# Kernel optimization log

Measured on AMD Instinct MI355X. Metric: run time of the kernel, lower is better.

## Reference

```python
import jax, jax.numpy as jnp
import numpy as np
from jax import lax

CHUNK = 32

def _l2norm(x, eps=1e-6):
    # matches fla l2norm: x / ||x||_2 along last dim
    return x * lax.rsqrt(jnp.sum(x * x, axis=-1, keepdims=True) + eps)

def _delta_rule_chunkwise(q, k, v, beta, chunk=CHUNK):
    b, h, L, dk = q.shape
    dv = v.shape[-1]
    pad = (-L) % chunk
    if pad:
        pw = ((0, 0), (0, 0), (0, pad), (0, 0))
        q = jnp.pad(q, pw); k = jnp.pad(k, pw); v = jnp.pad(v, pw)
        beta = jnp.pad(beta, ((0, 0), (0, 0), (0, pad)))
    Lp = L + pad
    n = Lp // chunk

    q = _l2norm(q)
    k = _l2norm(k)
    v = v * beta[..., None]
    k_beta = k * beta[..., None]

    # [b,h,n,c,d]
    rs = lambda t: t.reshape(b, h, n, chunk, t.shape[-1])
    qc, kc, vc, kbc = rs(q), rs(k), rs(v), rs(k_beta)

    idx = jnp.arange(chunk)
    strict_lower = (idx[:, None] > idx[None, :])           # used for inv
    lower_incl = (idx[:, None] >= idx[None, :])            # used for attn_local

    # inv = -(k_beta k^T), keep strictly-lower part only
    inv = jnp.where(strict_lower, -jnp.einsum('bhnid,bhnjd->bhnij', kbc, kc), 0.0)
    # sequential forward substitution: inv[i,:i] += inv[i,:] @ inv[:,:i]
    for i in range(1, chunk):
        row = inv[..., i, :]                                # [b,h,n,c]
        upd = jnp.einsum('bhnk,bhnkc->bhnc', row, inv)      # contributions from rows < i
        inv = inv.at[..., i, :].add(jnp.where(idx < i, upd, 0.0))
    inv = inv + jnp.eye(chunk, dtype=inv.dtype)

    u = jnp.einsum('bhnij,bhnjd->bhnid', inv, vc)           # [b,h,n,c,dv]
    w = jnp.einsum('bhnij,bhnjd->bhnid', inv, kbc)          # [b,h,n,c,dk]

    S0 = jnp.zeros((b, h, dk, dv), dtype=q.dtype)

    def step(S, blk):
        q_i, k_i, u_i0, w_i = blk
        attn = jnp.where(lower_incl, jnp.einsum('bhid,bhjd->bhij', q_i, k_i), 0.0)
        u_i = u_i0 - jnp.einsum('bhik,bhkd->bhid', w_i, S)
        o = jnp.einsum('bhik,bhkd->bhid', q_i, S) + jnp.einsum('bhij,bhjd->bhid', attn, u_i)
        S = S + jnp.einsum('bhci,bhcd->bhid', k_i, u_i)
        return S, o

    mv = lambda t: jnp.moveaxis(t, 2, 0)                    # [n,b,h,c,d]
    S, outs = lax.scan(step, S0, (mv(qc), mv(kc), mv(u), mv(w)))
    out = jnp.moveaxis(outs, 0, 2).reshape(b, h, Lp, dv)
    if pad:
        out = out[:, :, :L]
    return out, S

def setup_inputs() -> dict:
    key = jax.random.key(0)
    kq, kk, kv, kb = jax.random.split(key, 4)
    b, h, L, d = 2, 16, 4096, 128
    q = jax.random.normal(kq, (b, h, L, d), dtype=jnp.float32)
    k = jax.random.normal(kk, (b, h, L, d), dtype=jnp.float32)
    v = jax.random.normal(kv, (b, h, L, d), dtype=jnp.float32)
    beta = jax.random.uniform(kb, (b, h, L), dtype=jnp.float32)
    return {"q": q, "k": k, "v": v, "beta": beta}

def reference(q, k, v, beta):
    return _delta_rule_chunkwise(q, k, v, beta)
```

## Files before the change

### kernel.cpp

```cpp
#include <hip/hip_runtime.h>
#include <math.h>

#define BH   32
#define LSEQ 4096
#define DK   128
#define DV   128
#define CH   32
#define NC   (LSEQ/CH)

typedef float4 f4;
typedef unsigned short u16;
typedef __attribute__((ext_vector_type(8))) short  bf16x8;
typedef __attribute__((ext_vector_type(4))) float  f32x4;

#define MFMA16(a,b,c) __builtin_amdgcn_mfma_f32_16x16x32_bf16((a),(b),(c),0,0,0)

__device__ __forceinline__ float dot4(const f4 a, const f4 b) {
    return a.x*b.x + a.y*b.y + a.z*b.z + a.w*b.w;
}
__device__ __forceinline__ unsigned pk2(float a, float b) {
    unsigned ua = __builtin_bit_cast(unsigned, a);
    unsigned ub = __builtin_bit_cast(unsigned, b);
    ua = (ua + 0x7FFFu + ((ua >> 16) & 1u)) >> 16;
    ub = (ub + 0x7FFFu + ((ub >> 16) & 1u)) >> 16;
    return (ua & 0xFFFFu) | (ub << 16);
}
__device__ __forceinline__ u16 bf1(float a) {
    unsigned ua = __builtin_bit_cast(unsigned, a);
    ua = (ua + 0x7FFFu + ((ua >> 16) & 1u)) >> 16;
    return (u16)ua;
}

__global__ __launch_bounds__(256) void prep_kernel(
    const float* __restrict__ q, const float* __restrict__ k, float* __restrict__ v,
    const float* __restrict__ beta,
    u16* __restrict__ qb16, u16* __restrict__ wb16,
    u16* __restrict__ kT16, u16* __restrict__ A16)
{
    __shared__ u16 qn[CH][136];
    __shared__ u16 kn[CH][136];
    __shared__ u16 vT[DK][40];
    __shared__ u16 knT[DK][40];
    __shared__ float Ts[CH][33];
    __shared__ float Af[CH][33];
    __shared__ u16 Tb[CH][40];
    __shared__ float redq[CH][8], redk[CH][8];
    __shared__ float bet[CH], scq[CH], sck[CH];

    const int tid = threadIdx.x;
    const int hh  = blockIdx.x >> 7;
    const int c   = blockIdx.x & (NC-1);
    const size_t rowbase = (size_t)hh * LSEQ + (size_t)c * CH;
    const size_t base    = rowbase * DK;
    const size_t tb      = (size_t)(hh * NC + c);

    const int r = tid >> 3, sub = tid & 7, d0 = sub * 16;
    const int wid = tid >> 6, lane = tid & 63, quad = lane >> 4, m16 = lane & 15;

    f4 tq[4], tk[4], tv[4];
    float sq = 0.f, sk = 0.f;
#pragma unroll
    for (int m = 0; m < 4; ++m) {
        tq[m] = *(const f4*)(q + base + (size_t)r*DK + d0 + m*4);
        tk[m] = *(const f4*)(k + base + (size_t)r*DK + d0 + m*4);
        tv[m] = *(const f4*)(v + base + (size_t)r*DK + d0 + m*4);
        sq += dot4(tq[m], tq[m]);
        sk += dot4(tk[m], tk[m]);
    }
    redq[r][sub] = sq;
    redk[r][sub] = sk;
    if (tid < CH) bet[tid] = beta[rowbase + tid];
    __syncthreads();
    if (tid < CH) {
        float a = 0.f, b = 0.f;
#pragma unroll
        for (int j = 0; j < 8; ++j) { a += redq[tid][j]; b += redk[tid][j]; }
        scq[tid] = 1.0f / sqrtf(a + 1e-6f);
        sck[tid] = 1.0f / sqrtf(b + 1e-6f);
    }
    __syncthreads();
    const float aq = scq[r], ak = sck[r];
#pragma unroll
    for (int m = 0; m < 4; ++m) {
        tq[m].x *= aq; tq[m].y *= aq; tq[m].z *= aq; tq[m].w *= aq;
        tk[m].x *= ak; tk[m].y *= ak; tk[m].z *= ak; tk[m].w *= ak;
    }
    {
        uint4 p0, p1;
        p0.x = pk2(tq[0].x,tq[0].y); p0.y = pk2(tq[0].z,tq[0].w);
        p0.z = pk2(tq[1].x,tq[1].y); p0.w = pk2(tq[1].z,tq[1].w);
        p1.x = pk2(tq[2].x,tq[2].y); p1.y = pk2(tq[2].z,tq[2].w);
        p1.z = pk2(tq[3].x,tq[3].y); p1.w = pk2(tq[3].z,tq[3].w);
        *(uint4*)&qn[r][d0]     = p0;  *(uint4*)&qn[r][d0+8] = p1;
        *(uint4*)(qb16 + tb*4096 + (size_t)r*DK + d0)     = p0;
        *(uint4*)(qb16 + tb*4096 + (size_t)r*DK + d0 + 8) = p1;
        uint4 k0, k1;
        k0.x = pk2(tk[0].x,tk[0].y); k0.y = pk2(tk[0].z,tk[0].w);
        k0.z = pk2(tk[1].x,tk[1].y); k0.w = pk2(tk[1].z,tk[1].w);
        k1.x = pk2(tk[2].x,tk[2].y); k1.y = pk2(tk[2].z,tk[2].w);
        k1.z = pk2(tk[3].x,tk[3].y); k1.w = pk2(tk[3].z,tk[3].w);
        *(uint4*)&kn[r][d0]     = k0;  *(uint4*)&kn[r][d0+8] = k1;
    }
#pragma unroll
    for (int m = 0; m < 4; ++m) {
        knT[d0+m*4+0][r] = bf1(tk[m].x); knT[d0+m*4+1][r] = bf1(tk[m].y);
        knT[d0+m*4+2][r] = bf1(tk[m].z); knT[d0+m*4+3][r] = bf1(tk[m].w);
        vT [d0+m*4+0][r] = bf1(tv[m].x); vT [d0+m*4+1][r] = bf1(tv[m].y);
        vT [d0+m*4+2][r] = bf1(tv[m].z); vT [d0+m*4+3][r] = bf1(tv[m].w);
    }
    __syncthreads();

    {
        const int d = tid >> 1, jh = (tid & 1) * 16;
        uint4 z0 = *(const uint4*)&knT[d][jh];
        uint4 z1 = *(const uint4*)&knT[d][jh+8];
        *(uint4*)(kT16 + tb*4096 + (size_t)d*32 + jh)     = z0;
        *(uint4*)(kT16 + tb*4096 + (size_t)d*32 + jh + 8) = z1;
    }
    {
        const int ti = wid >> 1, tj = wid & 1;
        f32x4 aA = {0.f,0.f,0.f,0.f}, aG = {0.f,0.f,0.f,0.f};
#pragma unroll
        for (int ks = 0; ks < 4; ++ks) {
            bf16x8 xq = *(const bf16x8*)&qn[ti*16+m16][ks*32 + quad*8];
            bf16x8 xk = *(const bf16x8*)&kn[ti*16+m16][ks*32 + quad*8];
            bf16x8 yk = *(const bf16x8*)&kn[tj*16+m16][ks*32 + quad*8];
            aA = MFMA16(xq, yk, aA);
            aG = MFMA16(xk, yk, aG);
        }
#pragma unroll
        for (int reg = 0; reg < 4; ++reg) {
            Af[ti*16 + quad*4 + reg][tj*16 + m16] = aA[reg];
            Ts[ti*16 + quad*4 + reg][tj*16 + m16] = aG[reg];
        }
    }
    __syncthreads();

    {
        const int i = r, j0 = sub * 4;
        float a[4];
#pragma unroll
        for (int jj = 0; jj < 4; ++jj)
            a[jj] = (j0+jj <= i) ? Af[i][j0+jj] : 0.f;
        uint2 pa; pa.x = pk2(a[0], a[1]); pa.y = pk2(a[2], a[3]);
        *(uint2*)(A16 + tb*1024 + (size_t)i*32 + j0) = pa;
        const float bi = bet[i];
#pragma unroll
        for (int jj = 0; jj < 4; ++jj) {
            const int j = j0 + jj;
            const float gv = Ts[i][j];
            Ts[i][j] = (j < i) ? -bi * gv : 0.f;
        }
    }
    __syncthreads();

    if (tid < 32) {
        float rr[32];
#pragma unroll
        for (int i = 0; i < 32; ++i) rr[i] = Ts[i][tid];
#pragma unroll
        for (int i = 1; i < 32; ++i) {
            float t = 0.f;
#pragma unroll
            for (int kk = 0; kk < i; ++kk)
                t += __shfl(rr[i], kk) * rr[kk];
            rr[i] += t;
        }
        const float bj = bet[tid];
#pragma unroll
        for (int i = 0; i < 32; ++i)
            Ts[i][tid] = ((i == tid) ? 1.0f : rr[i]) * bj;
    }
    __syncthreads();
    {
        const int i = r, j0 = sub * 4;
        uint2 p; p.x = pk2(Ts[i][j0], Ts[i][j0+1]); p.y = pk2(Ts[i][j0+2], Ts[i][j0+3]);
        *(uint2*)&Tb[i][j0] = p;
    }
    __syncthreads();

#pragma unroll
    for (int dt = 0; dt < 2; ++dt)
#pragma unroll
    for (int it = 0; it < 2; ++it) {
        const int drow = wid*32 + dt*16 + m16;
        bf16x8 av  = *(const bf16x8*)&vT[drow][quad*8];
        bf16x8 ak2 = *(const bf16x8*)&knT[drow][quad*8];
        bf16x8 bT  = *(const bf16x8*)&Tb[it*16 + m16][quad*8];
        f32x4 aU = {0.f,0.f,0.f,0.f}, aW = {0.f,0.f,0.f,0.f};
        aU = MFMA16(av,  bT, aU);
        aW = MFMA16(ak2, bT, aW);
        const int ii = it*16 + m16;
        const int dd = wid*32 + dt*16 + quad*4;
        f4 us; us.x = aU[0]; us.y = aU[1]; us.z = aU[2]; us.w = aU[3];
        *(f4*)(v + base + (size_t)ii*DK + dd) = us;
        uint2 pw; pw.x = pk2(-aW[0], -aW[1]); pw.y = pk2(-aW[2], -aW[3]);
        *(uint2*)(wb16 + tb*4096 + (size_t)ii*DK + dd) = pw;
    }
}

__global__ __launch_bounds__(256) void scan_kernel(
    const u16* __restrict__ qb16, const u16* __restrict__ wb16,
    const u16* __restrict__ kT16, const u16* __restrict__ A16,
    const float* __restrict__ u0, float* __restrict__ out)
{
    __shared__ u16 qb[2][CH][136];
    __shared__ u16 wb[2][CH][136];
    __shared__ u16 kT[DK][40];
    __shared__ u16 Ab[CH][40];
    __shared__ u16 ST[16][136];
    __shared__ u16 uT[16][40];

    const int tid  = threadIdx.x;
    const int hh   = blockIdx.x & (BH-1);
    const int g    = blockIdx.x >> 5;
    const int wid  = tid >> 6;
    const int lane = tid & 63;
    const int quad = lane >> 4;
    const int m16  = lane & 15;

    const int srow = tid >> 3, sd0 = (tid & 7) * 16;
    const int kd = tid >> 1, kjh = (tid & 1) * 16;
    const int aj = (tid & 7) * 4;

    for (int i = tid; i < 16*136; i += 256) ((u16*)ST)[i] = 0;

    f32x4 S0 = {0.f,0.f,0.f,0.f}, S1 = {0.f,0.f,0.f,0.f};

    uint4 pq0, pq1, pw0, pw1, pk0, pk1; uint2 pa;
    float pu0 = 0.f, pu1 = 0.f, pu2 = 0.f, pu3 = 0.f;
    {
        const size_t tb = (size_t)(hh * NC);
        const u16* qg = qb16 + tb*4096;
        const u16* wg = wb16 + tb*4096;
        const u16* kg = kT16 + tb*4096;
        const u16* Ag = A16  + tb*1024;
        pq0 = *(const uint4*)(qg + (size_t)srow*DK + sd0);
        pq1 = *(const uint4*)(qg + (size_t)srow*DK + sd0 + 8);
        pw0 = *(const uint4*)(wg + (size_t)srow*DK + sd0);
        pw1 = *(const uint4*)(wg + (size_t)srow*DK + sd0 + 8);
        pk0 = *(const uint4*)(kg + (size_t)kd*32 + kjh);
        pk1 = *(const uint4*)(kg + (size_t)kd*32 + kjh + 8);
        pa  = *(const uint2*)(Ag + (size_t)srow*32 + aj);
        if (wid < 2) {
            const float* up = u0 + ((size_t)hh*LSEQ + wid*16 + quad*4)*DK + g*16 + m16;
            pu0 = up[0]; pu1 = up[DK]; pu2 = up[2*DK]; pu3 = up[3*DK];
        }
    }
    __syncthreads();

    for (int c = 0; c < NC; ++c) {
        const int buf = c & 1;
        *(uint4*)&qb[buf][srow][sd0]   = pq0;  *(uint4*)&qb[buf][srow][sd0+8] = pq1;
        *(uint4*)&wb[buf][srow][sd0]   = pw0;  *(uint4*)&wb[buf][srow][sd0+8] = pw1;
        __syncthreads();
        *(uint4*)&kT[kd][kjh]  = pk0;  *(uint4*)&kT[kd][kjh+8] = pk1;
        *(uint2*)&Ab[srow][aj] = pa;

        f32x4 acc;
        if (wid < 2) { acc.x = pu0; acc.y = pu1; acc.z = pu2; acc.w = pu3; }
        else         { acc.x = 0.f; acc.y = 0.f; acc.z = 0.f; acc.w = 0.f; }

        if (c + 1 < NC) {
            const size_t tb = (size_t)(hh*NC + c + 1);
            const u16* qg = qb16 + tb*4096;
            const u16* wg = wb16 + tb*4096;
            const u16* kg = kT16 + tb*4096;
            const u16* Ag = A16  + tb*1024;
            pq0 = *(const uint4*)(qg + (size_t)srow*DK + sd0);
            pq1 = *(const uint4*)(qg + (size_t)srow*DK + sd0 + 8);
            pw0 = *(const uint4*)(wg + (size_t)srow*DK + sd0);
            pw1 = *(const uint4*)(wg + (size_t)srow*DK + sd0 + 8);
            pk0 = *(const uint4*)(kg + (size_t)kd*32 + kjh);
            pk1 = *(const uint4*)(kg + (size_t)kd*32 + kjh + 8);
            pa  = *(const uint2*)(Ag + (size_t)srow*32 + aj);
            if (wid < 2) {
                const float* up = u0 + ((size_t)hh*LSEQ + (size_t)(c+1)*CH + wid*16 + quad*4)*DK
                                     + g*16 + m16;
                pu0 = up[0]; pu1 = up[DK]; pu2 = up[2*DK]; pu3 = up[3*DK];
            }
        }

        if (wid < 2) {
#pragma unroll
            for (int ks = 0; ks < 4; ++ks) {
                bf16x8 af = *(const bf16x8*)&wb[buf][wid*16 + m16][ks*32 + quad*8];
                bf16x8 bf = *(const bf16x8*)&ST[m16][ks*32 + quad*8];
                acc = MFMA16(af, bf, acc);
            }
            uint2 p; p.x = pk2(acc.x, acc.y); p.y = pk2(acc.z, acc.w);
            *(uint2*)&uT[m16][wid*16 + quad*4] = p;
        } else {
            const int tile = wid - 2;
#pragma unroll
            for (int ks = 0; ks < 4; ++ks) {
                bf16x8 af = *(const bf16x8*)&qb[buf][tile*16 + m16][ks*32 + quad*8];
                bf16x8 bf = *(const bf16x8*)&ST[m16][ks*32 + quad*8];
                acc = MFMA16(af, bf, acc);
            }
        }
        __syncthreads();

        bf16x8 ub = *(const bf16x8*)&uT[m16][quad*8];
        if (wid >= 2) {
            const int tile = wid - 2;
            bf16x8 af = *(const bf16x8*)&Ab[tile*16 + m16][quad*8];
            acc = MFMA16(af, ub, acc);
            float* op = out + ((size_t)hh*LSEQ + (size_t)c*CH + tile*16 + quad*4)*DV
                            + g*16 + m16;
            op[0] = acc.x; op[DV] = acc.y; op[2*DV] = acc.z; op[3*DV] = acc.w;
        }
        {
            bf16x8 a0 = *(const bf16x8*)&kT[wid*32 + m16][quad*8];
            bf16x8 a1 = *(const bf16x8*)&kT[wid*32 + 16 + m16][quad*8];
            S0 = MFMA16(a0, ub, S0);
            S1 = MFMA16(a1, ub, S1);
            uint2 p0; p0.x = pk2(S0.x, S0.y); p0.y = pk2(S0.z, S0.w);
            uint2 p1; p1.x = pk2(S1.x, S1.y); p1.y = pk2(S1.z, S1.w);
            *(uint2*)&ST[m16][wid*32 + quad*4]      = p0;
            *(uint2*)&ST[m16][wid*32 + 16 + quad*4] = p1;
        }
        __syncthreads();
    }

    {
        float* sp = out + (size_t)BH*LSEQ*DV
                        + ((size_t)hh*DK + wid*32 + quad*4)*DV + g*16 + m16;
        sp[0] = S0.x; sp[DV] = S0.y; sp[2*DV] = S0.z; sp[3*DV] = S0.w;
        float* sq = sp + (size_t)16*DV;
        sq[0] = S1.x; sq[DV] = S1.y; sq[2*DV] = S1.z; sq[3*DV] = S1.w;
    }
}

extern "C" void kernel_launch(void* const* d_in, const int* in_sizes, int n_in,
                              void* d_out, int out_size, void* d_ws, size_t ws_size,
                              hipStream_t stream) {
    (void)in_sizes; (void)n_in; (void)out_size; (void)ws_size;
    const float* q = (const float*)d_in[0];
    const float* k = (const float*)d_in[1];
    float* v = (float*)d_in[2];
    const float* beta = (const float*)d_in[3];
    float* out = (float*)d_out;

    const size_t NE = (size_t)BH * LSEQ * DK;
    u16* qb16 = (u16*)d_ws;
    u16* wb16 = qb16 + NE;
    u16* kT16 = wb16 + NE;
    u16* A16  = kT16 + NE;

    prep_kernel<<<dim3(BH*NC), dim3(256), 0, stream>>>(q, k, v, beta, qb16, wb16, kT16, A16);
    scan_kernel<<<dim3(8*BH), dim3(256), 0, stream>>>(qb16, wb16, kT16, A16, v, out);
}
```

Baseline: 395.2 us.

## Restructure scan kernel to one barrier per chunk with register-resident fragments

The sequential chunk scan is rewritten so every wave recomputes the u correction redundantly and passes it between lanes with shuffles rather than through LDS. This cuts the per-chunk barriers from three to one. The k and q/A fragments are loaded straight from global memory into registers one chunk ahead, and the w and u tiles are prefetched three chunks ahead into double-buffered, swizzled LDS. Only two waves now hold the state S, four tiles each. In exchange the u MFMAs are duplicated across all four waves, register pressure rises, and launch_bounds caps occupancy at one block.

```diff
diff --git a/kernel.cpp b/kernel.cpp
--- a/kernel.cpp
+++ b/kernel.cpp
@@ -199,17 +199,14 @@
     }
 }
 
-__global__ __launch_bounds__(256) void scan_kernel(
+__global__ __launch_bounds__(256, 1) void scan_kernel(
     const u16* __restrict__ qb16, const u16* __restrict__ wb16,
     const u16* __restrict__ kT16, const u16* __restrict__ A16,
     const float* __restrict__ u0, float* __restrict__ out)
 {
-    __shared__ u16 qb[2][CH][136];
-    __shared__ u16 wb[2][CH][136];
-    __shared__ u16 kT[DK][40];
-    __shared__ u16 Ab[CH][40];
-    __shared__ u16 ST[16][136];
-    __shared__ u16 uT[16][40];
+    __shared__ u16   wbc[2][16][CH][8];
+    __shared__ u16   STc[2][16][16][8];
+    __shared__ float uIT[2][16][36];
 
     const int tid  = threadIdx.x;
     const int hh   = blockIdx.x & (BH-1);
@@ -219,117 +216,148 @@
     const int quad = lane >> 4;
     const int m16  = lane & 15;
 
-    const int srow = tid >> 3, sd0 = (tid & 7) * 16;
-    const int kd = tid >> 1, kjh = (tid & 1) * 16;
-    const int aj = (tid & 7) * 4;
-
-    for (int i = tid; i < 16*136; i += 256) ((u16*)ST)[i] = 0;
-
+    const int srow = tid >> 3;
+    const int spl  = (tid & 7) * 2;
+    const int um   = (tid & 7) * 2;
+
+    const u16* qg = qb16 + (size_t)hh * NC * 4096;
+    const u16* wg = wb16 + (size_t)hh * NC * 4096;
+    const u16* kg = kT16 + (size_t)hh * NC * 4096;
+    const u16* Ag = A16  + (size_t)hh * NC * 1024;
+    const float* ug = u0 + (size_t)hh * LSEQ * DK + g * 16;
+
+    uint4 Ow0, Ow1, Ew0, Ew1; float2 Ou, Eu;
+    bf16x8 F0 = {}, F1 = {}, F2 = {}, F3 = {}, AF = {};
     f32x4 S0 = {0.f,0.f,0.f,0.f}, S1 = {0.f,0.f,0.f,0.f};
-
-    uint4 pq0, pq1, pw0, pw1, pk0, pk1; uint2 pa;
-    float pu0 = 0.f, pu1 = 0.f, pu2 = 0.f, pu3 = 0.f;
-    {
-        const size_t tb = (size_t)(hh * NC);
-        const u16* qg = qb16 + tb*4096;
-        const u16* wg = wb16 + tb*4096;
-        const u16* kg = kT16 + tb*4096;
-        const u16* Ag = A16  + tb*1024;
-        pq0 = *(const uint4*)(qg + (size_t)srow*DK + sd0);
-        pq1 = *(const uint4*)(qg + (size_t)srow*DK + sd0 + 8);
-        pw0 = *(const uint4*)(wg + (size_t)srow*DK + sd0);
-        pw1 = *(const uint4*)(wg + (size_t)srow*DK + sd0 + 8);
-        pk0 = *(const uint4*)(kg + (size_t)kd*32 + kjh);
-        pk1 = *(const uint4*)(kg + (size_t)kd*32 + kjh + 8);
-        pa  = *(const uint2*)(Ag + (size_t)srow*32 + aj);
-        if (wid < 2) {
-            const float* up = u0 + ((size_t)hh*LSEQ + wid*16 + quad*4)*DK + g*16 + m16;
-            pu0 = up[0]; pu1 = up[DK]; pu2 = up[2*DK]; pu3 = up[3*DK];
-        }
-    }
-    __syncthreads();
-
-    for (int c = 0; c < NC; ++c) {
-        const int buf = c & 1;
-        *(uint4*)&qb[buf][srow][sd0]   = pq0;  *(uint4*)&qb[buf][srow][sd0+8] = pq1;
-        *(uint4*)&wb[buf][srow][sd0]   = pw0;  *(uint4*)&wb[buf][srow][sd0+8] = pw1;
-        __syncthreads();
-        *(uint4*)&kT[kd][kjh]  = pk0;  *(uint4*)&kT[kd][kjh+8] = pk1;
-        *(uint2*)&Ab[srow][aj] = pa;
-
-        f32x4 acc;
-        if (wid < 2) { acc.x = pu0; acc.y = pu1; acc.z = pu2; acc.w = pu3; }
-        else         { acc.x = 0.f; acc.y = 0.f; acc.z = 0.f; acc.w = 0.f; }
-
-        if (c + 1 < NC) {
-            const size_t tb = (size_t)(hh*NC + c + 1);
-            const u16* qg = qb16 + tb*4096;
-            const u16* wg = wb16 + tb*4096;
-            const u16* kg = kT16 + tb*4096;
-            const u16* Ag = A16  + tb*1024;
-            pq0 = *(const uint4*)(qg + (size_t)srow*DK + sd0);
-            pq1 = *(const uint4*)(qg + (size_t)srow*DK + sd0 + 8);
-            pw0 = *(const uint4*)(wg + (size_t)srow*DK + sd0);
-            pw1 = *(const uint4*)(wg + (size_t)srow*DK + sd0 + 8);
-            pk0 = *(const uint4*)(kg + (size_t)kd*32 + kjh);
-            pk1 = *(const uint4*)(kg + (size_t)kd*32 + kjh + 8);
-            pa  = *(const uint2*)(Ag + (size_t)srow*32 + aj);
-            if (wid < 2) {
-                const float* up = u0 + ((size_t)hh*LSEQ + (size_t)(c+1)*CH + wid*16 + quad*4)*DK
-                                     + g*16 + m16;
-                pu0 = up[0]; pu1 = up[DK]; pu2 = up[2*DK]; pu3 = up[3*DK];
-            }
-        }
-
-        if (wid < 2) {
-#pragma unroll
-            for (int ks = 0; ks < 4; ++ks) {
-                bf16x8 af = *(const bf16x8*)&wb[buf][wid*16 + m16][ks*32 + quad*8];
-                bf16x8 bf = *(const bf16x8*)&ST[m16][ks*32 + quad*8];
-                acc = MFMA16(af, bf, acc);
-            }
-            uint2 p; p.x = pk2(acc.x, acc.y); p.y = pk2(acc.z, acc.w);
-            *(uint2*)&uT[m16][wid*16 + quad*4] = p;
-        } else {
-            const int tile = wid - 2;
-#pragma unroll
-            for (int ks = 0; ks < 4; ++ks) {
-                bf16x8 af = *(const bf16x8*)&qb[buf][tile*16 + m16][ks*32 + quad*8];
-                bf16x8 bf = *(const bf16x8*)&ST[m16][ks*32 + quad*8];
-                acc = MFMA16(af, bf, acc);
-            }
-        }
-        __syncthreads();
-
-        bf16x8 ub = *(const bf16x8*)&uT[m16][quad*8];
-        if (wid >= 2) {
-            const int tile = wid - 2;
-            bf16x8 af = *(const bf16x8*)&Ab[tile*16 + m16][quad*8];
-            acc = MFMA16(af, ub, acc);
-            float* op = out + ((size_t)hh*LSEQ + (size_t)c*CH + tile*16 + quad*4)*DV
-                            + g*16 + m16;
-            op[0] = acc.x; op[DV] = acc.y; op[2*DV] = acc.z; op[3*DV] = acc.w;
-        }
-        {
-            bf16x8 a0 = *(const bf16x8*)&kT[wid*32 + m16][quad*8];
-            bf16x8 a1 = *(const bf16x8*)&kT[wid*32 + 16 + m16][quad*8];
-            S0 = MFMA16(a0, ub, S0);
-            S1 = MFMA16(a1, ub, S1);
-            uint2 p0; p0.x = pk2(S0.x, S0.y); p0.y = pk2(S0.z, S0.w);
-            uint2 p1; p1.x = pk2(S1.x, S1.y); p1.y = pk2(S1.z, S1.w);
-            *(uint2*)&ST[m16][wid*32 + quad*4]      = p0;
-            *(uint2*)&ST[m16][wid*32 + 16 + quad*4] = p1;
-        }
-        __syncthreads();
-    }
-
-    {
+    f32x4 S2 = {0.f,0.f,0.f,0.f}, S3 = {0.f,0.f,0.f,0.f};
+
+#define PREF(P, cc) do { \
+    const u16* wp_ = wg + (size_t)(cc)*4096 + (size_t)srow*DK + (tid&7)*16; \
+    P##w0 = *(const uint4*)(wp_); \
+    P##w1 = *(const uint4*)(wp_ + 8); \
+    P##u  = *(const float2*)(ug + ((size_t)(cc)*CH + srow)*DK + um); \
+} while (0)
+
+#define STAGE(P, nb_) do { \
+    *(uint4*)&wbc[nb_][spl  ][srow][0] = P##w0; \
+    *(uint4*)&wbc[nb_][spl+1][srow][0] = P##w1; \
+    uIT[nb_][um  ][srow] = P##u.x; \
+    uIT[nb_][um+1][srow] = P##u.y; \
+} while (0)
+
+#define LOADFRAGS(cc) do { \
+    if (wid < 2) { \
+        const u16* kp_ = kg + (size_t)(cc)*4096 + (size_t)(wid*64 + m16)*32 + quad*8; \
+        F0 = *(const bf16x8*)(kp_); \
+        F1 = *(const bf16x8*)(kp_ + 16*32); \
+        F2 = *(const bf16x8*)(kp_ + 32*32); \
+        F3 = *(const bf16x8*)(kp_ + 48*32); \
+    } else { \
+        const u16* qp_ = qg + (size_t)(cc)*4096 + (size_t)((wid-2)*16 + m16)*DK + quad*8; \
+        F0 = *(const bf16x8*)(qp_); \
+        F1 = *(const bf16x8*)(qp_ + 32); \
+        F2 = *(const bf16x8*)(qp_ + 64); \
+        F3 = *(const bf16x8*)(qp_ + 96); \
+        AF = *(const bf16x8*)(Ag + (size_t)(cc)*1024 + (size_t)((wid-2)*16 + m16)*32 + quad*8); \
+    } \
+} while (0)
+
+    for (int i = tid; i < 16*16*8; i += 256) (&STc[0][0][0][0])[i] = 0;
+    PREF(O, 0);
+    STAGE(O, 0);
+    PREF(O, 1);
+    PREF(E, 2);
+    LOADFRAGS(0);
+    __syncthreads();
+
+#define BODY(c, b, P) do { \
+    const int nb = (b) ^ 1; \
+    STAGE(P, nb); \
+    { const int c3_ = ((c)+3 < NC) ? (c)+3 : NC-1; PREF(P, c3_); } \
+     \
+    f32x4 u0a = *(const f32x4*)&uIT[b][m16][quad*4]; \
+    f32x4 u1a = *(const f32x4*)&uIT[b][m16][16 + quad*4]; \
+    f32x4 u0b = {0.f,0.f,0.f,0.f}, u1b = {0.f,0.f,0.f,0.f}; \
+    bf16x8 sf0 = *(const bf16x8*)&STc[b][quad    ][m16][0]; \
+    bf16x8 sf1 = *(const bf16x8*)&STc[b][ 4+quad ][m16][0]; \
+    bf16x8 sf2 = *(const bf16x8*)&STc[b][ 8+quad ][m16][0]; \
+    bf16x8 sf3 = *(const bf16x8*)&STc[b][12+quad ][m16][0]; \
+    u0a = MFMA16(*(const bf16x8*)&wbc[b][quad    ][   m16][0], sf0, u0a); \
+    u1a = MFMA16(*(const bf16x8*)&wbc[b][quad    ][16+m16][0], sf0, u1a); \
+    u0b = MFMA16(*(const bf16x8*)&wbc[b][ 4+quad ][   m16][0], sf1, u0b); \
+    u1b = MFMA16(*(const bf16x8*)&wbc[b][ 4+quad ][16+m16][0], sf1, u1b); \
+    u0a = MFMA16(*(const bf16x8*)&wbc[b][ 8+quad ][   m16][0], sf2, u0a); \
+    u1a = MFMA16(*(const bf16x8*)&wbc[b][ 8+quad ][16+m16][0], sf2, u1a); \
+    u0b = MFMA16(*(const bf16x8*)&wbc[b][12+quad ][   m16][0], sf3, u0b); \
+    u1b = MFMA16(*(const bf16x8*)&wbc[b][12+quad ][16+m16][0], sf3, u1b); \
+    u0a[0]+=u0b[0]; u0a[1]+=u0b[1]; u0a[2]+=u0b[2]; u0a[3]+=u0b[3]; \
+    u1a[0]+=u1b[0]; u1a[1]+=u1b[1]; u1a[2]+=u1b[2]; u1a[3]+=u1b[3]; \
+     \
+    const unsigned W00 = pk2(u0a[0], u0a[1]), W01 = pk2(u0a[2], u0a[3]); \
+    const unsigned W10 = pk2(u1a[0], u1a[1]), W11 = pk2(u1a[2], u1a[3]); \
+    const int s0l_ = (2*(quad&1))*16 + m16, s1l_ = s0l_ + 16; \
+    union { unsigned w[4]; bf16x8 v; } uc_; \
+    { const unsigned a0_ = __shfl((int)W00, s0l_), b0_ = __shfl((int)W10, s0l_); \
+      const unsigned a1_ = __shfl((int)W01, s0l_), b1_ = __shfl((int)W11, s0l_); \
+      const unsigned a2_ = __shfl((int)W00, s1l_), b2_ = __shfl((int)W10, s1l_); \
+      const unsigned a3_ = __shfl((int)W01, s1l_), b3_ = __shfl((int)W11, s1l_); \
+      const bool hi_ = (quad >= 2); \
+      uc_.w[0] = hi_ ? b0_ : a0_; uc_.w[1] = hi_ ? b1_ : a1_; \
+      uc_.w[2] = hi_ ? b2_ : a2_; uc_.w[3] = hi_ ? b3_ : a3_; } \
+    const bf16x8 ub_ = uc_.v; \
+    if (wid < 2) { \
+         \
+        const int db_ = wid * 64; \
+        S0 = MFMA16(F0, ub_, S0); \
+        S1 = MFMA16(F1, ub_, S1); \
+        S2 = MFMA16(F2, ub_, S2); \
+        S3 = MFMA16(F3, ub_, S3); \
+        uint2 p_; \
+        p_.x = pk2(S0[0],S0[1]); p_.y = pk2(S0[2],S0[3]); \
+        *(uint2*)&STc[nb][(db_>>3)   + (quad>>1)][m16][4*(quad&1)] = p_; \
+        p_.x = pk2(S1[0],S1[1]); p_.y = pk2(S1[2],S1[3]); \
+        *(uint2*)&STc[nb][(db_>>3)+2 + (quad>>1)][m16][4*(quad&1)] = p_; \
+        p_.x = pk2(S2[0],S2[1]); p_.y = pk2(S2[2],S2[3]); \
+        *(uint2*)&STc[nb][(db_>>3)+4 + (quad>>1)][m16][4*(quad&1)] = p_; \
+        p_.x = pk2(S3[0],S3[1]); p_.y = pk2(S3[2],S3[3]); \
+        *(uint2*)&STc[nb][(db_>>3)+6 + (quad>>1)][m16][4*(quad&1)] = p_; \
+    } else { \
+         \
+        f32x4 Za = {0.f,0.f,0.f,0.f}, Zb = {0.f,0.f,0.f,0.f}; \
+        Za = MFMA16(F0, sf0, Za); \
+        Zb = MFMA16(F1, sf1, Zb); \
+        Za = MFMA16(F2, sf2, Za); \
+        Zb = MFMA16(F3, sf3, Zb); \
+        Za[0]+=Zb[0]; Za[1]+=Zb[1]; Za[2]+=Zb[2]; Za[3]+=Zb[3]; \
+        Za = MFMA16(AF, ub_, Za); \
+        float* op_ = out + ((size_t)hh*LSEQ + (size_t)(c)*CH + (wid-2)*16 + quad*4)*DV \
+                         + g*16 + m16; \
+        op_[0] = Za[0]; op_[DV] = Za[1]; op_[2*DV] = Za[2]; op_[3*DV] = Za[3]; \
+    } \
+    { const int c1_ = ((c)+1 < NC) ? (c)+1 : NC-1; LOADFRAGS(c1_); } \
+    __syncthreads(); \
+} while (0)
+
+    for (int c = 0; c < NC; c += 2) {
+        BODY(c,     0, O);
+        BODY(c + 1, 1, E);
+    }
+
+    if (wid < 2) {
         float* sp = out + (size_t)BH*LSEQ*DV
-                        + ((size_t)hh*DK + wid*32 + quad*4)*DV + g*16 + m16;
-        sp[0] = S0.x; sp[DV] = S0.y; sp[2*DV] = S0.z; sp[3*DV] = S0.w;
-        float* sq = sp + (size_t)16*DV;
-        sq[0] = S1.x; sq[DV] = S1.y; sq[2*DV] = S1.z; sq[3*DV] = S1.w;
-    }
+                        + ((size_t)hh*DK + wid*64 + quad*4)*DV + g*16 + m16;
+        sp[0] = S0[0]; sp[DV] = S0[1]; sp[2*DV] = S0[2]; sp[3*DV] = S0[3];
+        sp += (size_t)16*DV;
+        sp[0] = S1[0]; sp[DV] = S1[1]; sp[2*DV] = S1[2]; sp[3*DV] = S1[3];
+        sp += (size_t)16*DV;
+        sp[0] = S2[0]; sp[DV] = S2[1]; sp[2*DV] = S2[2]; sp[3*DV] = S2[3];
+        sp += (size_t)16*DV;
+        sp[0] = S3[0]; sp[DV] = S3[1]; sp[2*DV] = S3[2]; sp[3*DV] = S3[3];
+    }
+#undef BODY
+#undef LOADFRAGS
+#undef STAGE
+#undef PREF
 }
 
 extern "C" void kernel_launch(void* const* d_in, const int* in_sizes, int n_in,
```

New measurement: 378.3 us. -4.3%, faster.

## Rewrite scan as single-wave blocks using register fragments and MFMA-ready layouts

Applied to the files above, without the earlier changes.

The prep kernel now writes q, w, kT and A in a pre-swizzled MFMA fragment order, so the scan kernel can load operands straight into registers with contiguous per-lane loads. The scan kernel drops to one 64-thread wave per block. It keeps the state S in accumulator registers, shares u across lanes with shuffles, and round-trips only S through a small swizzled LDS buffer, which removes all block-wide barriers from the sequential chunk loop. It also prefetches the next chunk's fragments between MFMA groups and uses the hardware bf16 pack instruction. The trade-off is higher register pressure and only 4x fewer threads per block to cover memory latency.

```diff
diff --git a/kernel.cpp b/kernel.cpp
--- a/kernel.cpp
+++ b/kernel.cpp
@@ -29,6 +29,11 @@
     unsigned ua = __builtin_bit_cast(unsigned, a);
     ua = (ua + 0x7FFFu + ((ua >> 16) & 1u)) >> 16;
     return (u16)ua;
+}
+__device__ __forceinline__ unsigned cvtpk(float a, float b) {
+    unsigned r;
+    asm("v_cvt_pk_bf16_f32 %0, %1, %2" : "=v"(r) : "v"(a), "v"(b));
+    return r;
 }
 
 __global__ __launch_bounds__(256) void prep_kernel(
@@ -92,8 +97,9 @@
         p1.x = pk2(tq[2].x,tq[2].y); p1.y = pk2(tq[2].z,tq[2].w);
         p1.z = pk2(tq[3].x,tq[3].y); p1.w = pk2(tq[3].z,tq[3].w);
         *(uint4*)&qn[r][d0]     = p0;  *(uint4*)&qn[r][d0+8] = p1;
-        *(uint4*)(qb16 + tb*4096 + (size_t)r*DK + d0)     = p0;
-        *(uint4*)(qb16 + tb*4096 + (size_t)r*DK + d0 + 8) = p1;
+        const int qf = ((r>>4)*4 + (sub>>1))*512 + ((r&15) + (sub&1)*32)*8;
+        *(uint4*)(qb16 + tb*4096 + qf)       = p0;
+        *(uint4*)(qb16 + tb*4096 + qf + 128) = p1;
         uint4 k0, k1;
         k0.x = pk2(tk[0].x,tk[0].y); k0.y = pk2(tk[0].z,tk[0].w);
         k0.z = pk2(tk[1].x,tk[1].y); k0.w = pk2(tk[1].z,tk[1].w);
@@ -114,8 +120,9 @@
         const int d = tid >> 1, jh = (tid & 1) * 16;
         uint4 z0 = *(const uint4*)&knT[d][jh];
         uint4 z1 = *(const uint4*)&knT[d][jh+8];
-        *(uint4*)(kT16 + tb*4096 + (size_t)d*32 + jh)     = z0;
-        *(uint4*)(kT16 + tb*4096 + (size_t)d*32 + jh + 8) = z1;
+        const int kf = (d>>4)*512 + ((d&15) + (tid&1)*32)*8;
+        *(uint4*)(kT16 + tb*4096 + kf)       = z0;
+        *(uint4*)(kT16 + tb*4096 + kf + 128) = z1;
     }
     {
         const int ti = wid >> 1, tj = wid & 1;
@@ -143,7 +150,8 @@
         for (int jj = 0; jj < 4; ++jj)
             a[jj] = (j0+jj <= i) ? Af[i][j0+jj] : 0.f;
         uint2 pa; pa.x = pk2(a[0], a[1]); pa.y = pk2(a[2], a[3]);
-        *(uint2*)(A16 + tb*1024 + (size_t)i*32 + j0) = pa;
+        const int af = (i>>4)*512 + ((i&15) + (sub>>1)*16)*8 + (sub&1)*4;
+        *(uint2*)(A16 + tb*1024 + af) = pa;
         const float bi = bet[i];
 #pragma unroll
         for (int jj = 0; jj < 4; ++jj) {
@@ -195,141 +203,142 @@
         f4 us; us.x = aU[0]; us.y = aU[1]; us.z = aU[2]; us.w = aU[3];
         *(f4*)(v + base + (size_t)ii*DK + dd) = us;
         uint2 pw; pw.x = pk2(-aW[0], -aW[1]); pw.y = pk2(-aW[2], -aW[3]);
-        *(uint2*)(wb16 + tb*4096 + (size_t)ii*DK + dd) = pw;
-    }
-}
-
-__global__ __launch_bounds__(256) void scan_kernel(
+        const int wf = (it*4 + wid)*512 + (m16 + (dt*2 + (quad>>1))*16)*8 + (quad&1)*4;
+        *(uint2*)(wb16 + tb*4096 + wf) = pw;
+    }
+}
+
+__global__ __launch_bounds__(64) void scan_kernel(
     const u16* __restrict__ qb16, const u16* __restrict__ wb16,
     const u16* __restrict__ kT16, const u16* __restrict__ A16,
     const float* __restrict__ u0, float* __restrict__ out)
 {
-    __shared__ u16 qb[2][CH][136];
-    __shared__ u16 wb[2][CH][136];
-    __shared__ u16 kT[DK][40];
-    __shared__ u16 Ab[CH][40];
-    __shared__ u16 ST[16][136];
-    __shared__ u16 uT[16][40];
-
-    const int tid  = threadIdx.x;
-    const int hh   = blockIdx.x & (BH-1);
-    const int g    = blockIdx.x >> 5;
-    const int wid  = tid >> 6;
-    const int lane = tid & 63;
-    const int quad = lane >> 4;
-    const int m16  = lane & 15;
-
-    const int srow = tid >> 3, sd0 = (tid & 7) * 16;
-    const int kd = tid >> 1, kjh = (tid & 1) * 16;
-    const int aj = (tid & 7) * 4;
-
-    for (int i = tid; i < 16*136; i += 256) ((u16*)ST)[i] = 0;
-
-    f32x4 S0 = {0.f,0.f,0.f,0.f}, S1 = {0.f,0.f,0.f,0.f};
-
-    uint4 pq0, pq1, pw0, pw1, pk0, pk1; uint2 pa;
-    float pu0 = 0.f, pu1 = 0.f, pu2 = 0.f, pu3 = 0.f;
-    {
-        const size_t tb = (size_t)(hh * NC);
-        const u16* qg = qb16 + tb*4096;
-        const u16* wg = wb16 + tb*4096;
-        const u16* kg = kT16 + tb*4096;
-        const u16* Ag = A16  + tb*1024;
-        pq0 = *(const uint4*)(qg + (size_t)srow*DK + sd0);
-        pq1 = *(const uint4*)(qg + (size_t)srow*DK + sd0 + 8);
-        pw0 = *(const uint4*)(wg + (size_t)srow*DK + sd0);
-        pw1 = *(const uint4*)(wg + (size_t)srow*DK + sd0 + 8);
-        pk0 = *(const uint4*)(kg + (size_t)kd*32 + kjh);
-        pk1 = *(const uint4*)(kg + (size_t)kd*32 + kjh + 8);
-        pa  = *(const uint2*)(Ag + (size_t)srow*32 + aj);
-        if (wid < 2) {
-            const float* up = u0 + ((size_t)hh*LSEQ + wid*16 + quad*4)*DK + g*16 + m16;
-            pu0 = up[0]; pu1 = up[DK]; pu2 = up[2*DK]; pu3 = up[3*DK];
-        }
-    }
-    __syncthreads();
+    __shared__ u16 STl[16*128];
+
+    const int lane = threadIdx.x;
+    const int quad = lane >> 4, m16 = lane & 15;
+    const int hh = blockIdx.x & 31, g = blockIdx.x >> 5;
+
+    const u16* wg = wb16 + (size_t)hh * NC * 4096 + lane*8;
+    const u16* qg = qb16 + (size_t)hh * NC * 4096 + lane*8;
+    const u16* kg = kT16 + (size_t)hh * NC * 4096 + lane*8;
+    const u16* Ag = A16  + (size_t)hh * NC * 1024 + lane*8;
+    const float* ug = u0 + (size_t)hh * LSEQ * DK + (size_t)(quad*4)*DK + g*16 + m16;
+    float* og = out + (size_t)hh * LSEQ * DV + (size_t)(quad*4)*DV + g*16 + m16;
+
+    const int swz = (m16 & 7) << 3;
+
+    bf16x8 WA[8], KA[8], QA[8], AA[2];
+    f32x4 U0r[2];
+    f32x4 SA[8];
+    bf16x8 SB[4];
+#pragma unroll
+    for (int t = 0; t < 8; ++t) SA[t] = (f32x4){0.f,0.f,0.f,0.f};
+#pragma unroll
+    for (int ks = 0; ks < 4; ++ks) SB[ks] = (bf16x8){};
+
+#define LOADWU(cc) do { \
+    const u16* wp_ = wg + (size_t)(cc)*4096; \
+    _Pragma("unroll") \
+    for (int f = 0; f < 8; ++f) WA[f] = *(const bf16x8*)(wp_ + f*512); \
+    const float* up_ = ug + (size_t)(cc)*CH*DK; \
+    _Pragma("unroll") \
+    for (int r2 = 0; r2 < 4; ++r2) { \
+        U0r[0][r2] = up_[(size_t)r2*DK]; \
+        U0r[1][r2] = up_[(size_t)(16+r2)*DK]; } \
+} while (0)
+#define LOADK(cc) do { \
+    const u16* kp_ = kg + (size_t)(cc)*4096; \
+    _Pragma("unroll") \
+    for (int f = 0; f < 8; ++f) KA[f] = *(const bf16x8*)(kp_ + f*512); \
+} while (0)
+#define LOADQ(cc) do { \
+    const u16* qp_ = qg + (size_t)(cc)*4096; \
+    _Pragma("unroll") \
+    for (int f = 0; f < 8; ++f) QA[f] = *(const bf16x8*)(qp_ + f*512); \
+    const u16* ap_ = Ag + (size_t)(cc)*1024; \
+    AA[0] = *(const bf16x8*)(ap_); \
+    AA[1] = *(const bf16x8*)(ap_ + 512); \
+} while (0)
+
+    LOADWU(0); LOADK(0); LOADQ(0);
 
     for (int c = 0; c < NC; ++c) {
-        const int buf = c & 1;
-        *(uint4*)&qb[buf][srow][sd0]   = pq0;  *(uint4*)&qb[buf][srow][sd0+8] = pq1;
-        *(uint4*)&wb[buf][srow][sd0]   = pw0;  *(uint4*)&wb[buf][srow][sd0+8] = pw1;
-        __syncthreads();
-        *(uint4*)&kT[kd][kjh]  = pk0;  *(uint4*)&kT[kd][kjh+8] = pk1;
-        *(uint2*)&Ab[srow][aj] = pa;
-
-        f32x4 acc;
-        if (wid < 2) { acc.x = pu0; acc.y = pu1; acc.z = pu2; acc.w = pu3; }
-        else         { acc.x = 0.f; acc.y = 0.f; acc.z = 0.f; acc.w = 0.f; }
-
-        if (c + 1 < NC) {
-            const size_t tb = (size_t)(hh*NC + c + 1);
-            const u16* qg = qb16 + tb*4096;
-            const u16* wg = wb16 + tb*4096;
-            const u16* kg = kT16 + tb*4096;
-            const u16* Ag = A16  + tb*1024;
-            pq0 = *(const uint4*)(qg + (size_t)srow*DK + sd0);
-            pq1 = *(const uint4*)(qg + (size_t)srow*DK + sd0 + 8);
-            pw0 = *(const uint4*)(wg + (size_t)srow*DK + sd0);
-            pw1 = *(const uint4*)(wg + (size_t)srow*DK + sd0 + 8);
-            pk0 = *(const uint4*)(kg + (size_t)kd*32 + kjh);
-            pk1 = *(const uint4*)(kg + (size_t)kd*32 + kjh + 8);
-            pa  = *(const uint2*)(Ag + (size_t)srow*32 + aj);
-            if (wid < 2) {
-                const float* up = u0 + ((size_t)hh*LSEQ + (size_t)(c+1)*CH + wid*16 + quad*4)*DK
-                                     + g*16 + m16;
-                pu0 = up[0]; pu1 = up[DK]; pu2 = up[2*DK]; pu3 = up[3*DK];
-            }
-        }
-
-        if (wid < 2) {
-#pragma unroll
-            for (int ks = 0; ks < 4; ++ks) {
-                bf16x8 af = *(const bf16x8*)&wb[buf][wid*16 + m16][ks*32 + quad*8];
-                bf16x8 bf = *(const bf16x8*)&ST[m16][ks*32 + quad*8];
-                acc = MFMA16(af, bf, acc);
-            }
-            uint2 p; p.x = pk2(acc.x, acc.y); p.y = pk2(acc.z, acc.w);
-            *(uint2*)&uT[m16][wid*16 + quad*4] = p;
-        } else {
-            const int tile = wid - 2;
-#pragma unroll
-            for (int ks = 0; ks < 4; ++ks) {
-                bf16x8 af = *(const bf16x8*)&qb[buf][tile*16 + m16][ks*32 + quad*8];
-                bf16x8 bf = *(const bf16x8*)&ST[m16][ks*32 + quad*8];
-                acc = MFMA16(af, bf, acc);
-            }
-        }
-        __syncthreads();
-
-        bf16x8 ub = *(const bf16x8*)&uT[m16][quad*8];
-        if (wid >= 2) {
-            const int tile = wid - 2;
-            bf16x8 af = *(const bf16x8*)&Ab[tile*16 + m16][quad*8];
-            acc = MFMA16(af, ub, acc);
-            float* op = out + ((size_t)hh*LSEQ + (size_t)c*CH + tile*16 + quad*4)*DV
-                            + g*16 + m16;
-            op[0] = acc.x; op[DV] = acc.y; op[2*DV] = acc.z; op[3*DV] = acc.w;
-        }
+        const int cn = (c + 1 < NC) ? c + 1 : c;
+
+        f32x4 ua0 = U0r[0], ua1 = U0r[1];
+        f32x4 ub0 = {0.f,0.f,0.f,0.f}, ub1 = {0.f,0.f,0.f,0.f};
+        ua0 = MFMA16(WA[0], SB[0], ua0);  ub0 = MFMA16(WA[1], SB[1], ub0);
+        ua0 = MFMA16(WA[2], SB[2], ua0);  ub0 = MFMA16(WA[3], SB[3], ub0);
+        ua1 = MFMA16(WA[4], SB[0], ua1);  ub1 = MFMA16(WA[5], SB[1], ub1);
+        ua1 = MFMA16(WA[6], SB[2], ua1);  ub1 = MFMA16(WA[7], SB[3], ub1);
+        ua0 += ub0;  ua1 += ub1;
+
+        LOADWU(cn);
+
+        const unsigned Wa0 = cvtpk(ua0[0], ua0[1]), Wa1 = cvtpk(ua0[2], ua0[3]);
+        const unsigned Wb0 = cvtpk(ua1[0], ua1[1]), Wb1 = cvtpk(ua1[2], ua1[3]);
+        const int s0l = ((quad & 1) << 5) + m16, s1l = s0l + 16;
+        union { unsigned w[4]; bf16x8 v; } uc;
         {
-            bf16x8 a0 = *(const bf16x8*)&kT[wid*32 + m16][quad*8];
-            bf16x8 a1 = *(const bf16x8*)&kT[wid*32 + 16 + m16][quad*8];
-            S0 = MFMA16(a0, ub, S0);
-            S1 = MFMA16(a1, ub, S1);
-            uint2 p0; p0.x = pk2(S0.x, S0.y); p0.y = pk2(S0.z, S0.w);
-            uint2 p1; p1.x = pk2(S1.x, S1.y); p1.y = pk2(S1.z, S1.w);
-            *(uint2*)&ST[m16][wid*32 + quad*4]      = p0;
-            *(uint2*)&ST[m16][wid*32 + 16 + quad*4] = p1;
-        }
-        __syncthreads();
-    }
-
-    {
-        float* sp = out + (size_t)BH*LSEQ*DV
-                        + ((size_t)hh*DK + wid*32 + quad*4)*DV + g*16 + m16;
-        sp[0] = S0.x; sp[DV] = S0.y; sp[2*DV] = S0.z; sp[3*DV] = S0.w;
-        float* sq = sp + (size_t)16*DV;
-        sq[0] = S1.x; sq[DV] = S1.y; sq[2*DV] = S1.z; sq[3*DV] = S1.w;
-    }
+            const unsigned a0 = __shfl((int)Wa0, s0l), b0 = __shfl((int)Wb0, s0l);
+            const unsigned a1 = __shfl((int)Wa1, s0l), b1 = __shfl((int)Wb1, s0l);
+            const unsigned a2 = __shfl((int)Wa0, s1l), b2 = __shfl((int)Wb0, s1l);
+            const unsigned a3 = __shfl((int)Wa1, s1l), b3 = __shfl((int)Wb1, s1l);
+            const bool hi = (quad >= 2);
+            uc.w[0] = hi ? b0 : a0; uc.w[1] = hi ? b1 : a1;
+            uc.w[2] = hi ? b2 : a2; uc.w[3] = hi ? b3 : a3;
+        }
+        const bf16x8 UB = uc.v;
+
+#pragma unroll
+        for (int t = 0; t < 8; ++t)
+            SA[t] = MFMA16(KA[t], UB, SA[t]);
+
+        LOADK(cn);
+
+        f32x4 za0 = {0.f,0.f,0.f,0.f}, zb0 = {0.f,0.f,0.f,0.f};
+        f32x4 za1 = {0.f,0.f,0.f,0.f}, zb1 = {0.f,0.f,0.f,0.f};
+        za0 = MFMA16(QA[0], SB[0], za0);  zb0 = MFMA16(QA[1], SB[1], zb0);
+        za0 = MFMA16(QA[2], SB[2], za0);  zb0 = MFMA16(QA[3], SB[3], zb0);
+        za1 = MFMA16(QA[4], SB[0], za1);  zb1 = MFMA16(QA[5], SB[1], zb1);
+        za1 = MFMA16(QA[6], SB[2], za1);  zb1 = MFMA16(QA[7], SB[3], zb1);
+        za0 += zb0;  za1 += zb1;
+        za0 = MFMA16(AA[0], UB, za0);
+        za1 = MFMA16(AA[1], UB, za1);
+        {
+            float* o0 = og + (size_t)c * CH * DV;
+            o0[0] = za0[0]; o0[DV] = za0[1]; o0[2*DV] = za0[2]; o0[3*DV] = za0[3];
+            float* o1 = o0 + (size_t)16 * DV;
+            o1[0] = za1[0]; o1[DV] = za1[1]; o1[2*DV] = za1[2]; o1[3*DV] = za1[3];
+        }
+
+        LOADQ(cn);
+
+#pragma unroll
+        for (int t = 0; t < 8; ++t) {
+            uint2 p;
+            p.x = cvtpk(SA[t][0], SA[t][1]);
+            p.y = cvtpk(SA[t][2], SA[t][3]);
+            *(uint2*)&STl[(m16*128 + t*16 + quad*4) ^ swz] = p;
+        }
+#pragma unroll
+        for (int ks = 0; ks < 4; ++ks)
+            SB[ks] = *(const bf16x8*)&STl[(m16*128 + ks*32 + quad*8) ^ swz];
+    }
+
+    {
+        float* sg = out + (size_t)BH*LSEQ*DV
+                        + ((size_t)hh*DK + quad*4)*DV + g*16 + m16;
+#pragma unroll
+        for (int t = 0; t < 8; ++t) {
+            float* sp = sg + (size_t)t * 16 * DV;
+            sp[0] = SA[t][0]; sp[DV] = SA[t][1]; sp[2*DV] = SA[t][2]; sp[3*DV] = SA[t][3];
+        }
+    }
+#undef LOADQ
+#undef LOADK
+#undef LOADWU
 }
 
 extern "C" void kernel_launch(void* const* d_in, const int* in_sizes, int n_in,
@@ -349,5 +358,5 @@
     u16* A16  = kT16 + NE;
 
     prep_kernel<<<dim3(BH*NC), dim3(256), 0, stream>>>(q, k, v, beta, qb16, wb16, kT16, A16);
-    scan_kernel<<<dim3(8*BH), dim3(256), 0, stream>>>(qb16, wb16, kT16, A16, v, out);
-}
+    scan_kernel<<<dim3(256), dim3(64), 0, stream>>>(qb16, wb16, kT16, A16, v, out);
+}
```

After: 411.5 us. 1.04x slower.
